# Optimization experiments

Hardware: AMD Instinct MI355X
Metric: run time of the kernel (lower is better)

## Reference

```python
import jax, jax.numpy as jnp
import numpy as np

N = 100_000   # nodes
E = 3_200_000 # edges
G = 128       # graphs in batch
H = 32        # hidden_dim
PI = float(np.pi)


def setup_inputs() -> dict:
    key = jax.random.key(0)
    ks = jax.random.split(key, 18)
    p = lambda k, s: (jax.random.normal(k, s, dtype=jnp.float32) * 0.1)
    x = jax.random.normal(ks[0], (N, 1), dtype=jnp.float32)
    edge_index = jax.random.randint(ks[1], (2, E), 0, N, dtype=jnp.int32)
    batch = jnp.sort(jax.random.randint(ks[2], (N,), 0, G, dtype=jnp.int32))
    return dict(
        x=x, edge_index=edge_index, batch=batch,
        W1=p(ks[3], (1, H)),  b1=jnp.zeros((H,), jnp.float32),
        W2=p(ks[4], (H, H)),  b2=jnp.zeros((H,), jnp.float32),
        W3=p(ks[5], (H, H)),  b3=jnp.zeros((H,), jnp.float32),
        Wt1=p(ks[6], (H, 32)), bt1=jnp.zeros((32,), jnp.float32),
        Wt2=p(ks[7], (32, 1)), bt2=jnp.zeros((1,), jnp.float32),
        Wg1=p(ks[8], (H, 32)), bg1=jnp.zeros((32,), jnp.float32),
        Wg2=p(ks[9], (32, 2)), bg2=jnp.zeros((2,), jnp.float32),
    )


def _gcn_norm(edge_index):
    # PyG GCNConv default: add self-loops, symmetric normalization.
    loop = jnp.arange(N, dtype=edge_index.dtype)
    src = jnp.concatenate([edge_index[0], loop])
    dst = jnp.concatenate([edge_index[1], loop])
    deg = jax.ops.segment_sum(jnp.ones_like(dst, dtype=jnp.float32), dst, num_segments=N)
    dinv = jnp.where(deg > 0, jax.lax.rsqrt(jnp.maximum(deg, 1.0)), 0.0)
    norm = dinv[src] * dinv[dst]  # [E+N]
    return src, dst, norm


def _gcn_conv(x, W, b, src, dst, norm):
    h = x @ W                                  # [N, out]
    msg = h[src] * norm[:, None]               # gather + scale  [E+N, out]
    return jax.ops.segment_sum(msg, dst, num_segments=N) + b


def _forward(x, W1, b1, W2, b2, W3, b3, Wt1, bt1, Wt2, bt2, Wg1, bg1, Wg2, bg2,
             edge_index, batch):
    src, dst, norm = _gcn_norm(edge_index)
    x = jax.nn.relu(_gcn_conv(x, W1, b1, src, dst, norm))
    x = jax.nn.relu(_gcn_conv(x, W2, b2, src, dst, norm))
    h = jax.nn.relu(_gcn_conv(x, W3, b3, src, dst, norm))
    # theta head per node
    theta = PI * jax.nn.sigmoid(jax.nn.relu(h @ Wt1 + bt1) @ Wt2 + bt2)[:, 0]  # [N]
    # global mean pool per graph
    counts = jax.ops.segment_sum(jnp.ones((N,), jnp.float32), batch, num_segments=G)
    gsum = jax.ops.segment_sum(h, batch, num_segments=G)
    gemb = gsum / jnp.maximum(counts, 1.0)[:, None]                            # [G, H]
    beta_gamma = 2.0 * PI * jax.nn.sigmoid(jax.nn.relu(gemb @ Wg1 + bg1) @ Wg2 + bg2)  # [G, 2]
    return theta, beta_gamma


def reference(x, edge_index, batch, W1, b1, W2, b2, W3, b3,
              Wt1, bt1, Wt2, bt2, Wg1, bg1, Wg2, bg2):
    return _forward(x, W1, b1, W2, b2, W3, b3, Wt1, bt1, Wt2, bt2,
                    Wg1, bg1, Wg2, bg2, edge_index, batch)
```

## Files before the change

### kernel.cpp

```cpp
#include <hip/hip_runtime.h>
#include <hip/hip_bf16.h>

#define PI_F 3.14159265358979323846f
#define NBLK 256
#define BSH 8
#define BSZ 256
#define SCAP 10240

static inline size_t align256(size_t x) { return (x + 255) & ~size_t(255); }

typedef float v2f __attribute__((ext_vector_type(2)));

__device__ __forceinline__ unsigned bfpack(float a, float b) {
    unsigned lo = (__float_as_uint(a) + 0x8000u) >> 16;
    unsigned hi = (__float_as_uint(b) + 0x8000u) & 0xFFFF0000u;
    return lo | hi;
}

__device__ __forceinline__ void f8acc(uint2 q, float rs, float acc[8]) {
    v2f l0 = __builtin_amdgcn_cvt_pk_f32_fp8(q.x, false);
    v2f h0 = __builtin_amdgcn_cvt_pk_f32_fp8(q.x, true);
    v2f l1 = __builtin_amdgcn_cvt_pk_f32_fp8(q.y, false);
    v2f h1 = __builtin_amdgcn_cvt_pk_f32_fp8(q.y, true);
    acc[0] += rs * l0.x; acc[1] += rs * l0.y; acc[2] += rs * h0.x; acc[3] += rs * h0.y;
    acc[4] += rs * l1.x; acc[5] += rs * l1.y; acc[6] += rs * h1.x; acc[7] += rs * h1.y;
}


__global__ void __launch_bounds__(1024) count_kernel(
                             const int* __restrict__ dst, int* __restrict__ C,
                             int E, int CHUNK, int NB2) {
    extern __shared__ int hist[];
    for (int i = threadIdx.x; i < NB2; i += 1024) hist[i] = 0;
    __syncthreads();
    int s0 = blockIdx.x * CHUNK, s1 = min(s0 + CHUNK, E);
    for (int e = s0 + threadIdx.x; e < s1; e += 1024)
        atomicAdd(&hist[dst[e] >> BSH], 1);
    __syncthreads();
    for (int i = threadIdx.x; i < NB2; i += 1024)
        C[(size_t)blockIdx.x * NB2 + i] = hist[i];
}

__global__ void scan_blocks_kernel(int* __restrict__ C, int* __restrict__ colsum, int NB2) {
    __shared__ int s[256];
    int k = blockIdx.x;
    int b = threadIdx.x;
    int v = C[(size_t)b * NB2 + k];
    s[b] = v;
    __syncthreads();
    for (int off = 1; off < 256; off <<= 1) {
        int w = (b >= off) ? s[b - off] : 0;
        __syncthreads();
        s[b] += w;
        __syncthreads();
    }
    C[(size_t)b * NB2 + k] = s[b] - v;
    if (b == 255) colsum[k] = s[255];
}

__global__ void scan_totals_kernel(const int* __restrict__ colsum, int* __restrict__ bbase,
                                   int NB2, int E) {
    __shared__ int s[256];
    __shared__ int running;
    if (threadIdx.x == 0) running = 0;
    __syncthreads();
    for (int base = 0; base < NB2; base += 256) {
        int i = base + threadIdx.x;
        int v = (i < NB2) ? colsum[i] : 0;
        s[threadIdx.x] = v;
        __syncthreads();
        for (int off = 1; off < 256; off <<= 1) {
            int w = (threadIdx.x >= (unsigned)off) ? s[threadIdx.x - off] : 0;
            __syncthreads();
            s[threadIdx.x] += w;
            __syncthreads();
        }
        if (i < NB2) bbase[i] = running + s[threadIdx.x] - v;
        __syncthreads();
        if (threadIdx.x == 255) running += s[255];
        __syncthreads();
    }
    if (threadIdx.x == 0) bbase[NB2] = E;
}

__global__ void __launch_bounds__(1024) scatter_kernel(
                               const int* __restrict__ src, const int* __restrict__ dst,
                               const int* __restrict__ C, const int* __restrict__ bbase,
                               unsigned* __restrict__ bkt_data, int E, int CHUNK, int NB2) {
    extern __shared__ int ofs[];
    for (int i = threadIdx.x; i < NB2; i += 1024)
        ofs[i] = bbase[i] + C[(size_t)blockIdx.x * NB2 + i];
    __syncthreads();
    int s0 = blockIdx.x * CHUNK, s1 = min(s0 + CHUNK, E);
    for (int e = s0 + threadIdx.x; e < s1; e += 1024) {
        int d = dst[e];
        int p = atomicAdd(&ofs[d >> BSH], 1);
        bkt_data[p] = ((unsigned)(d & (BSZ - 1)) << 17) | (unsigned)src[e];
    }
}

__global__ void __launch_bounds__(512) csr_build_kernel(
                                 const unsigned* __restrict__ bkt_data, const int* __restrict__ bbase,
                                 const float* __restrict__ x,
                                 unsigned* __restrict__ csr, int* __restrict__ e_start,
                                 float* __restrict__ dinv, float* __restrict__ xd,
                                 int N, int NB2) {
    __shared__ unsigned sdata[SCAP];
    __shared__ int hist[256];
    __shared__ int scn[256];
    __shared__ int bump[256];
    int tid = threadIdx.x;
    int b = blockIdx.x;
    int g0 = bbase[b], g1 = bbase[b + 1];
    int cnt = g1 - g0;
    bool fits = (cnt <= SCAP);
    if (tid < 256) hist[tid] = 0;
    __syncthreads();
    for (int i = tid; i < cnt; i += 512) {
        unsigned pk = bkt_data[g0 + i];
        if (fits) sdata[i] = pk;
        atomicAdd(&hist[pk >> 17], 1);
    }
    __syncthreads();
    int orig = (tid < 256) ? hist[tid] : 0;
    if (tid < 256) scn[tid] = orig;
    __syncthreads();
    for (int off = 1; off < 256; off <<= 1) {
        int w = (tid >= off && tid < 256) ? scn[tid - off] : 0;
        __syncthreads();
        if (tid < 256) scn[tid] += w;
        __syncthreads();
    }
    if (tid < 256) {
        int excl = scn[tid] - orig;
        bump[tid] = g0 + excl;
        int node = b * BSZ + tid;
        if (node < N) {
            float dv = rsqrtf((float)(orig + 1));
            dinv[node] = dv;
            xd[node] = x[node] * dv;
            e_start[node] = g0 + excl;
        }
    }
    if (b == NB2 - 1 && tid == 0) e_start[N] = g1;
    __syncthreads();
    for (int i = tid; i < cnt; i += 512) {
        unsigned pk = fits ? sdata[i] : bkt_data[g0 + i];
        int p = atomicAdd(&bump[pk >> 17], 1);
        csr[p] = pk & 0x1FFFFu;
    }
}


__device__ __forceinline__ void mm32_8(const float* __restrict__ sW, const float vr[8],
                                       int sub, int lane, float o[8]) {
    const float4* sW4 = (const float4*)sW;
    int base = lane & ~3;
#pragma unroll
    for (int r = 0; r < 4; r++) {
#pragma unroll
        for (int i = 0; i < 8; i++) {
            float vk = __shfl(vr[i], base | r, 64);
            int k = r * 8 + i;
            float4 w0 = sW4[k * 8 + sub * 2];
            float4 w1 = sW4[k * 8 + sub * 2 + 1];
            o[0] += vk * w0.x; o[1] += vk * w0.y; o[2] += vk * w0.z; o[3] += vk * w0.w;
            o[4] += vk * w1.x; o[5] += vk * w1.y; o[6] += vk * w1.z; o[7] += vk * w1.w;
        }
    }
}

__device__ __forceinline__ void store_f8(unsigned char* __restrict__ u8, float* __restrict__ uscale,
                                         int d, int sub, const float o[8]) {
    float am = 0.f;
#pragma unroll
    for (int i = 0; i < 8; i++) am = fmaxf(am, fabsf(o[i]));
    am = fmaxf(am, __shfl_xor(am, 1, 64));
    am = fmaxf(am, __shfl_xor(am, 2, 64));
    float rm = fmaxf(am, 1e-20f);
    float sc = 128.f / rm;
    unsigned w0 = 0, w1 = 0;
    w0 = __builtin_amdgcn_cvt_pk_fp8_f32(o[0] * sc, o[1] * sc, w0, false);
    w0 = __builtin_amdgcn_cvt_pk_fp8_f32(o[2] * sc, o[3] * sc, w0, true);
    w1 = __builtin_amdgcn_cvt_pk_fp8_f32(o[4] * sc, o[5] * sc, w1, false);
    w1 = __builtin_amdgcn_cvt_pk_fp8_f32(o[6] * sc, o[7] * sc, w1, true);
    uint2 st; st.x = w0; st.y = w1;
    ((uint2*)u8)[(size_t)d * 4 + sub] = st;
    if (sub == 0) uscale[d] = rm * (1.f / 128.f);
}

__global__ void __launch_bounds__(256) agg1_kernel(
                            const float* __restrict__ xd, const int* __restrict__ e_start,
                            const unsigned* __restrict__ csr, const float* __restrict__ dinv,
                            const float* __restrict__ W1, const float* __restrict__ b1,
                            const float* __restrict__ W2,
                            unsigned char* __restrict__ u8o, float* __restrict__ uso, int n) {
    __shared__ float sW2[1024];
    __shared__ float sW1[32], sb1[32];
    for (int i = threadIdx.x; i < 1024; i += 256) sW2[i] = W2[i];
    if (threadIdx.x < 32) { sW1[threadIdx.x] = W1[threadIdx.x]; sb1[threadIdx.x] = b1[threadIdx.x]; }
    __syncthreads();
    int t = blockIdx.x * 256 + threadIdx.x;
    int d = t >> 2, sub = t & 3;
    int lane = threadIdx.x & 63;
    if (d >= n) return;
    int e0 = e_start[d];
    int cnt = e_start[d + 1] - e0;
    float s = 0.f;
    int j = sub;
    for (; j + 8 <= cnt; j += 8) {
        int i0 = (int)csr[e0 + j], i1 = (int)csr[e0 + j + 4];
        s += xd[i0]; s += xd[i1];
    }
    for (; j < cnt; j += 4) s += xd[(int)csr[e0 + j]];
    s += __shfl_xor(s, 1, 64);
    s += __shfl_xor(s, 2, 64);
    float dv = dinv[d];
    float tt = dv * (s + xd[d]);
    float vr[8];
#pragma unroll
    for (int i = 0; i < 8; i++) vr[i] = fmaxf(tt * sW1[sub * 8 + i] + sb1[sub * 8 + i], 0.f);
    float o[8];
#pragma unroll
    for (int i = 0; i < 8; i++) o[i] = 0.f;
    mm32_8(sW2, vr, sub, lane, o);
#pragma unroll
    for (int i = 0; i < 8; i++) o[i] *= dv;
    store_f8(u8o, uso, d, sub, o);
}

__device__ __forceinline__ void gather_f8(const unsigned char* __restrict__ u8,
                                          const float* __restrict__ uscale,
                                          const unsigned* __restrict__ csr,
                                          int e0, int cnt, int d, int sub, float acc[8]) {
#pragma unroll
    for (int i = 0; i < 8; i++) acc[i] = 0.f;
    const uint2* rows = (const uint2*)u8;
    int j = 0;
    for (; j + 4 <= cnt; j += 4) {
        int i0 = (int)csr[e0 + j],     i1 = (int)csr[e0 + j + 1];
        int i2 = (int)csr[e0 + j + 2], i3 = (int)csr[e0 + j + 3];
        float r0 = uscale[i0], r1 = uscale[i1], r2 = uscale[i2], r3 = uscale[i3];
        uint2 q0 = rows[(size_t)i0 * 4 + sub];
        uint2 q1 = rows[(size_t)i1 * 4 + sub];
        uint2 q2 = rows[(size_t)i2 * 4 + sub];
        uint2 q3 = rows[(size_t)i3 * 4 + sub];
        f8acc(q0, r0, acc); f8acc(q1, r1, acc); f8acc(q2, r2, acc); f8acc(q3, r3, acc);
    }
    for (; j < cnt; j++) {
        int i0 = (int)csr[e0 + j];
        float r0 = uscale[i0];
        uint2 q0 = rows[(size_t)i0 * 4 + sub];
        f8acc(q0, r0, acc);
    }
    float rs = uscale[d];
    uint2 qs = rows[(size_t)d * 4 + sub];
    f8acc(qs, rs, acc);
}

__global__ void __launch_bounds__(256) agg2_kernel(
                            const unsigned char* __restrict__ u8, const float* __restrict__ uscale,
                            const int* __restrict__ e_start, const unsigned* __restrict__ csr,
                            const float* __restrict__ dinv, const float* __restrict__ bias,
                            const float* __restrict__ W,
                            unsigned char* __restrict__ o8, float* __restrict__ oscale, int n) {
    __shared__ float sW[1024];
    __shared__ float sb[32];
    for (int i = threadIdx.x; i < 1024; i += 256) sW[i] = W[i];
    if (threadIdx.x < 32) sb[threadIdx.x] = bias[threadIdx.x];
    __syncthreads();
    int t = blockIdx.x * 256 + threadIdx.x;
    int d = t >> 2, sub = t & 3;
    int lane = threadIdx.x & 63;
    if (d >= n) return;
    int e0 = e_start[d];
    int cnt = e_start[d + 1] - e0;
    float acc[8];
    gather_f8(u8, uscale, csr, e0, cnt, d, sub, acc);
    float dv = dinv[d];
    float vr[8];
#pragma unroll
    for (int i = 0; i < 8; i++) vr[i] = fmaxf(dv * acc[i] + sb[sub * 8 + i], 0.f);
    float o[8];
#pragma unroll
    for (int i = 0; i < 8; i++) o[i] = 0.f;
    mm32_8(sW, vr, sub, lane, o);
#pragma unroll
    for (int i = 0; i < 8; i++) o[i] *= dv;
    store_f8(o8, oscale, d, sub, o);
}

__global__ void __launch_bounds__(256) agg3_kernel(
                            const unsigned char* __restrict__ u8, const float* __restrict__ uscale,
                            const int* __restrict__ e_start, const unsigned* __restrict__ csr,
                            const float* __restrict__ dinv, const float* __restrict__ bias,
                            const float* __restrict__ Wt1, const float* __restrict__ bt1,
                            const float* __restrict__ Wt2, const float* __restrict__ bt2,
                            unsigned short* __restrict__ hb, float* __restrict__ theta, int n) {
    __shared__ float sW[1024];
    __shared__ float sb[32], sbt[32], sw2[32];
    for (int i = threadIdx.x; i < 1024; i += 256) sW[i] = Wt1[i];
    if (threadIdx.x < 32) {
        sb[threadIdx.x] = bias[threadIdx.x];
        sbt[threadIdx.x] = bt1[threadIdx.x];
        sw2[threadIdx.x] = Wt2[threadIdx.x];
    }
    __syncthreads();
    int t = blockIdx.x * 256 + threadIdx.x;
    int d = t >> 2, sub = t & 3;
    int lane = threadIdx.x & 63;
    if (d >= n) return;
    int e0 = e_start[d];
    int cnt = e_start[d + 1] - e0;
    float acc[8];
    gather_f8(u8, uscale, csr, e0, cnt, d, sub, acc);
    float dv = dinv[d];
    float vr[8];
#pragma unroll
    for (int i = 0; i < 8; i++) vr[i] = fmaxf(dv * acc[i] + sb[sub * 8 + i], 0.f);
    unsigned ow[4];
#pragma unroll
    for (int i2 = 0; i2 < 4; i2++) ow[i2] = bfpack(vr[2 * i2], vr[2 * i2 + 1]);
    ((uint4*)hb)[(size_t)d * 4 + sub] = *(uint4*)&ow[0];
    float o[8];
#pragma unroll
    for (int i = 0; i < 8; i++) o[i] = 0.f;
    mm32_8(sW, vr, sub, lane, o);
    float tl = 0.f;
#pragma unroll
    for (int i = 0; i < 8; i++)
        tl += fmaxf(o[i] + sbt[sub * 8 + i], 0.f) * sw2[sub * 8 + i];
    tl += __shfl_xor(tl, 1, 64);
    tl += __shfl_xor(tl, 2, 64);
    if (sub == 0) theta[d] = PI_F / (1.f + __expf(-(tl + bt2[0])));
}


__global__ void gb_kernel(const int* __restrict__ batch, int* __restrict__ gstart,
                          int n, int G) {
    int i = blockIdx.x * 256 + threadIdx.x;
    if (i >= n) return;
    int g = batch[i];
    if (i == 0) {
        for (int gg = 0; gg <= g; gg++) gstart[gg] = 0;
    } else {
        int gp = batch[i - 1];
        for (int gg = gp + 1; gg <= g; gg++) gstart[gg] = i;
    }
    if (i == n - 1) {
        for (int gg = g + 1; gg <= G; gg++) gstart[gg] = n;
    }
}

__global__ void __launch_bounds__(512) bg_kernel(
                          const unsigned short* __restrict__ hb, const int* __restrict__ gstart,
                          const float* __restrict__ Wg1, const float* __restrict__ bg1v,
                          const float* __restrict__ Wg2, const float* __restrict__ bg2v,
                          float* __restrict__ out, int G) {
    __shared__ float sW[1024];
    __shared__ float part[8][32];
    for (int i = threadIdx.x; i < 1024; i += 512) sW[i] = Wg1[i];
    int g = blockIdx.x;
    int s = gstart[g], e = gstart[g + 1];
    int w = threadIdx.x >> 6;
    int lane = threadIdx.x & 63;
    int f = lane & 31, h = lane >> 5;
    float a = 0.f;
    for (int i = s + (w << 1) + h; i < e; i += 16)
        a += __uint_as_float((unsigned)hb[((size_t)i << 5) + f] << 16);
    a += __shfl_xor(a, 32, 64);
    if (h == 0) part[w][f] = a;
    __syncthreads();
    if (w == 0) {
        float hv = 0.f;
#pragma unroll
        for (int p = 0; p < 8; p++) hv += part[p][f];
        hv /= fmaxf((float)(e - s), 1.f);
        int base = lane & 32;
        float acc = bg1v[f];
#pragma unroll
        for (int k = 0; k < 32; k++) acc += __shfl(hv, base | k, 64) * sW[k * 32 + f];
        acc = fmaxf(acc, 0.f);
        float p0 = acc * Wg2[f * 2 + 0];
        float p1 = acc * Wg2[f * 2 + 1];
#pragma unroll
        for (int m = 1; m < 32; m <<= 1) {
            p0 += __shfl_xor(p0, m, 64);
            p1 += __shfl_xor(p1, m, 64);
        }
        if (lane == 0) {
            out[g * 2 + 0] = 2.f * PI_F / (1.f + __expf(-(p0 + bg2v[0])));
            out[g * 2 + 1] = 2.f * PI_F / (1.f + __expf(-(p1 + bg2v[1])));
        }
    }
}


extern "C" void kernel_launch(void* const* d_in, const int* in_sizes, int n_in,
                              void* d_out, int out_size, void* d_ws, size_t ws_size,
                              hipStream_t stream) {
    const float* x   = (const float*)d_in[0];
    const int*   ei  = (const int*)d_in[1];
    const int* batch = (const int*)d_in[2];
    const float* W1  = (const float*)d_in[3];
    const float* b1  = (const float*)d_in[4];
    const float* W2  = (const float*)d_in[5];
    const float* b2  = (const float*)d_in[6];
    const float* W3  = (const float*)d_in[7];
    const float* b3  = (const float*)d_in[8];
    const float* Wt1 = (const float*)d_in[9];
    const float* bt1 = (const float*)d_in[10];
    const float* Wt2 = (const float*)d_in[11];
    const float* bt2 = (const float*)d_in[12];
    const float* Wg1 = (const float*)d_in[13];
    const float* bg1 = (const float*)d_in[14];
    const float* Wg2 = (const float*)d_in[15];
    const float* bg2 = (const float*)d_in[16];

    const int N = in_sizes[0];
    const int E = in_sizes[1] / 2;
    const int G = 128;
    const int* src = ei;
    const int* dst = ei + E;
    float* theta_out = (float*)d_out;
    float* bg_out = (float*)d_out + N;

    const int NB2 = (N + BSZ - 1) >> BSH;
    const int CHUNK = (E + NBLK - 1) / NBLK;

    char* w = (char*)d_ws;
    auto alloc = [&](size_t bytes) -> char* { char* p = w; w += align256(bytes); return p; };
    int*      C        = (int*)alloc((size_t)NBLK * NB2 * 4);
    int*      colsum   = (int*)alloc((size_t)NB2 * 4);
    int*      bbase    = (int*)alloc((size_t)(NB2 + 1) * 4);
    unsigned* bkt_data = (unsigned*)alloc((size_t)E * 4);
    unsigned* csr      = (unsigned*)alloc((size_t)E * 4);
    int*      e_start  = (int*)alloc((size_t)(N + 1) * 4);
    float*    dinv     = (float*)alloc((size_t)N * 4);
    float*    xd       = (float*)alloc((size_t)N * 4);
    unsigned char* u2  = (unsigned char*)alloc((size_t)N * 32);
    float*    us2      = (float*)alloc((size_t)N * 4);
    unsigned char* u3  = (unsigned char*)alloc((size_t)N * 32);
    float*    us3      = (float*)alloc((size_t)N * 4);
    unsigned short* hb = (unsigned short*)alloc((size_t)N * 64);
    int*      gstart   = (int*)alloc((size_t)(G + 1) * 4);

    size_t ldsB = (size_t)NB2 * 4;
    count_kernel<<<NBLK, 1024, ldsB, stream>>>(dst, C, E, CHUNK, NB2);
    scan_blocks_kernel<<<NB2, 256, 0, stream>>>(C, colsum, NB2);
    scan_totals_kernel<<<1, 256, 0, stream>>>(colsum, bbase, NB2, E);
    scatter_kernel<<<NBLK, 1024, ldsB, stream>>>(src, dst, C, bbase, bkt_data, E, CHUNK, NB2);
    csr_build_kernel<<<NB2, 512, 0, stream>>>(bkt_data, bbase, x, csr, e_start, dinv, xd, N, NB2);
    gb_kernel<<<(N + 255) / 256, 256, 0, stream>>>(batch, gstart, N, G);

    unsigned gridQ = (unsigned)(((size_t)N * 4 + 255) / 256);

    agg1_kernel<<<gridQ, 256, 0, stream>>>(xd, e_start, csr, dinv, W1, b1, W2, u2, us2, N);
    agg2_kernel<<<gridQ, 256, 0, stream>>>(u2, us2, e_start, csr, dinv, b2, W3, u3, us3, N);
    agg3_kernel<<<gridQ, 256, 0, stream>>>(u3, us3, e_start, csr, dinv, b3,
                                           Wt1, bt1, Wt2, bt2, hb, theta_out, N);

    bg_kernel<<<G, 512, 0, stream>>>(hb, gstart, Wg1, bg1, Wg2, bg2, bg_out, G);
}
```

Before: 287.8 us.

## Stage per-block CSR neighbor indices in LDS for aggregation kernels

Each aggregation kernel block now loads the contiguous CSR index range for its 64 destination nodes into shared memory with nontemporal loads, then gathers neighbors from LDS indices instead of re-reading global CSR per thread. The fp8 gather loop is unrolled to 8 neighbors to raise memory-level parallelism, with a fallback to the old global path when the range exceeds the LDS capacity. Output stores of hb and theta use nontemporal hints. It adds 12KB of LDS per block, which can reduce occupancy, and an extra barrier.

```diff
diff --git a/kernel.cpp b/kernel.cpp
--- a/kernel.cpp
+++ b/kernel.cpp
@@ -6,10 +6,12 @@
 #define BSH 8
 #define BSZ 256
 #define SCAP 10240
+#define SLDS 3072
 
 static inline size_t align256(size_t x) { return (x + 255) & ~size_t(255); }
 
 typedef float v2f __attribute__((ext_vector_type(2)));
+typedef unsigned uvec4 __attribute__((ext_vector_type(4)));
 
 __device__ __forceinline__ unsigned bfpack(float a, float b) {
     unsigned lo = (__float_as_uint(a) + 0x8000u) >> 16;
@@ -189,6 +191,21 @@
     if (sub == 0) uscale[d] = rm * (1.f / 128.f);
 }
 
+__device__ __forceinline__ bool stage_csr(const unsigned* __restrict__ csr,
+                                          const int* __restrict__ e_start,
+                                          int d0, int dEnd, int* sidx, int& E0) {
+    E0 = e_start[d0];
+    int E1 = e_start[dEnd];
+    int m = E1 - E0;
+    bool fits = (m <= SLDS);
+    if (fits) {
+        for (int i = threadIdx.x; i < m; i += 256)
+            sidx[i] = (int)__builtin_nontemporal_load(&csr[E0 + i]);
+    }
+    __syncthreads();
+    return fits;
+}
+
 __global__ void __launch_bounds__(256) agg1_kernel(
                             const float* __restrict__ xd, const int* __restrict__ e_start,
                             const unsigned* __restrict__ csr, const float* __restrict__ dinv,
@@ -197,22 +214,26 @@
                             unsigned char* __restrict__ u8o, float* __restrict__ uso, int n) {
     __shared__ float sW2[1024];
     __shared__ float sW1[32], sb1[32];
+    __shared__ int sidx[SLDS];
     for (int i = threadIdx.x; i < 1024; i += 256) sW2[i] = W2[i];
     if (threadIdx.x < 32) { sW1[threadIdx.x] = W1[threadIdx.x]; sb1[threadIdx.x] = b1[threadIdx.x]; }
-    __syncthreads();
-    int t = blockIdx.x * 256 + threadIdx.x;
-    int d = t >> 2, sub = t & 3;
+    int d0 = blockIdx.x * 64;
+    int dEnd = min(d0 + 64, n);
+    int E0;
+    bool fits = stage_csr(csr, e_start, d0, dEnd, sidx, E0);
+    int d = d0 + (threadIdx.x >> 2), sub = threadIdx.x & 3;
     int lane = threadIdx.x & 63;
     if (d >= n) return;
     int e0 = e_start[d];
     int cnt = e_start[d + 1] - e0;
+    int l0 = e0 - E0;
     float s = 0.f;
     int j = sub;
-    for (; j + 8 <= cnt; j += 8) {
-        int i0 = (int)csr[e0 + j], i1 = (int)csr[e0 + j + 4];
-        s += xd[i0]; s += xd[i1];
-    }
-    for (; j < cnt; j += 4) s += xd[(int)csr[e0 + j]];
+    if (fits) {
+        for (; j < cnt; j += 4) s += xd[sidx[l0 + j]];
+    } else {
+        for (; j < cnt; j += 4) s += xd[(int)csr[e0 + j]];
+    }
     s += __shfl_xor(s, 1, 64);
     s += __shfl_xor(s, 2, 64);
     float dv = dinv[d];
@@ -231,31 +252,48 @@
 
 __device__ __forceinline__ void gather_f8(const unsigned char* __restrict__ u8,
                                           const float* __restrict__ uscale,
+                                          const int* __restrict__ sidx, bool fits,
                                           const unsigned* __restrict__ csr,
-                                          int e0, int cnt, int d, int sub, float acc[8]) {
+                                          int e0, int l0, int cnt, int d, int sub, float acc[8]) {
 #pragma unroll
     for (int i = 0; i < 8; i++) acc[i] = 0.f;
     const uint2* rows = (const uint2*)u8;
     int j = 0;
-    for (; j + 4 <= cnt; j += 4) {
-        int i0 = (int)csr[e0 + j],     i1 = (int)csr[e0 + j + 1];
-        int i2 = (int)csr[e0 + j + 2], i3 = (int)csr[e0 + j + 3];
-        float r0 = uscale[i0], r1 = uscale[i1], r2 = uscale[i2], r3 = uscale[i3];
-        uint2 q0 = rows[(size_t)i0 * 4 + sub];
-        uint2 q1 = rows[(size_t)i1 * 4 + sub];
-        uint2 q2 = rows[(size_t)i2 * 4 + sub];
-        uint2 q3 = rows[(size_t)i3 * 4 + sub];
-        f8acc(q0, r0, acc); f8acc(q1, r1, acc); f8acc(q2, r2, acc); f8acc(q3, r3, acc);
-    }
-    for (; j < cnt; j++) {
-        int i0 = (int)csr[e0 + j];
-        float r0 = uscale[i0];
-        uint2 q0 = rows[(size_t)i0 * 4 + sub];
-        f8acc(q0, r0, acc);
-    }
-    float rs = uscale[d];
-    uint2 qs = rows[(size_t)d * 4 + sub];
-    f8acc(qs, rs, acc);
+    if (fits) {
+        for (; j + 8 <= cnt; j += 8) {
+            int id[8];
+#pragma unroll
+            for (int k = 0; k < 8; k++) id[k] = sidx[l0 + j + k];
+            float rs[8];
+#pragma unroll
+            for (int k = 0; k < 8; k++) rs[k] = uscale[id[k]];
+            uint2 q[8];
+#pragma unroll
+            for (int k = 0; k < 8; k++) q[k] = rows[(size_t)id[k] * 4 + sub];
+#pragma unroll
+            for (int k = 0; k < 8; k++) f8acc(q[k], rs[k], acc);
+        }
+        for (; j < cnt; j++) {
+            int i0 = sidx[l0 + j];
+            f8acc(rows[(size_t)i0 * 4 + sub], uscale[i0], acc);
+        }
+    } else {
+        for (; j + 4 <= cnt; j += 4) {
+            int i0 = (int)csr[e0 + j],     i1 = (int)csr[e0 + j + 1];
+            int i2 = (int)csr[e0 + j + 2], i3 = (int)csr[e0 + j + 3];
+            float r0 = uscale[i0], r1 = uscale[i1], r2 = uscale[i2], r3 = uscale[i3];
+            uint2 q0 = rows[(size_t)i0 * 4 + sub];
+            uint2 q1 = rows[(size_t)i1 * 4 + sub];
+            uint2 q2 = rows[(size_t)i2 * 4 + sub];
+            uint2 q3 = rows[(size_t)i3 * 4 + sub];
+            f8acc(q0, r0, acc); f8acc(q1, r1, acc); f8acc(q2, r2, acc); f8acc(q3, r3, acc);
+        }
+        for (; j < cnt; j++) {
+            int i0 = (int)csr[e0 + j];
+            f8acc(rows[(size_t)i0 * 4 + sub], uscale[i0], acc);
+        }
+    }
+    f8acc(rows[(size_t)d * 4 + sub], uscale[d], acc);
 }
 
 __global__ void __launch_bounds__(256) agg2_kernel(
@@ -266,17 +304,20 @@
                             unsigned char* __restrict__ o8, float* __restrict__ oscale, int n) {
     __shared__ float sW[1024];
     __shared__ float sb[32];
+    __shared__ int sidx[SLDS];
     for (int i = threadIdx.x; i < 1024; i += 256) sW[i] = W[i];
     if (threadIdx.x < 32) sb[threadIdx.x] = bias[threadIdx.x];
-    __syncthreads();
-    int t = blockIdx.x * 256 + threadIdx.x;
-    int d = t >> 2, sub = t & 3;
+    int d0 = blockIdx.x * 64;
+    int dEnd = min(d0 + 64, n);
+    int E0;
+    bool fits = stage_csr(csr, e_start, d0, dEnd, sidx, E0);
+    int d = d0 + (threadIdx.x >> 2), sub = threadIdx.x & 3;
     int lane = threadIdx.x & 63;
     if (d >= n) return;
     int e0 = e_start[d];
     int cnt = e_start[d + 1] - e0;
     float acc[8];
-    gather_f8(u8, uscale, csr, e0, cnt, d, sub, acc);
+    gather_f8(u8, uscale, sidx, fits, csr, e0, e0 - E0, cnt, d, sub, acc);
     float dv = dinv[d];
     float vr[8];
 #pragma unroll
@@ -299,29 +340,34 @@
                             unsigned short* __restrict__ hb, float* __restrict__ theta, int n) {
     __shared__ float sW[1024];
     __shared__ float sb[32], sbt[32], sw2[32];
+    __shared__ int sidx[SLDS];
     for (int i = threadIdx.x; i < 1024; i += 256) sW[i] = Wt1[i];
     if (threadIdx.x < 32) {
         sb[threadIdx.x] = bias[threadIdx.x];
         sbt[threadIdx.x] = bt1[threadIdx.x];
         sw2[threadIdx.x] = Wt2[threadIdx.x];
     }
-    __syncthreads();
-    int t = blockIdx.x * 256 + threadIdx.x;
-    int d = t >> 2, sub = t & 3;
+    int d0 = blockIdx.x * 64;
+    int dEnd = min(d0 + 64, n);
+    int E0;
+    bool fits = stage_csr(csr, e_start, d0, dEnd, sidx, E0);
+    int d = d0 + (threadIdx.x >> 2), sub = threadIdx.x & 3;
     int lane = threadIdx.x & 63;
     if (d >= n) return;
     int e0 = e_start[d];
     int cnt = e_start[d + 1] - e0;
     float acc[8];
-    gather_f8(u8, uscale, csr, e0, cnt, d, sub, acc);
+    gather_f8(u8, uscale, sidx, fits, csr, e0, e0 - E0, cnt, d, sub, acc);
     float dv = dinv[d];
     float vr[8];
 #pragma unroll
     for (int i = 0; i < 8; i++) vr[i] = fmaxf(dv * acc[i] + sb[sub * 8 + i], 0.f);
-    unsigned ow[4];
-#pragma unroll
-    for (int i2 = 0; i2 < 4; i2++) ow[i2] = bfpack(vr[2 * i2], vr[2 * i2 + 1]);
-    ((uint4*)hb)[(size_t)d * 4 + sub] = *(uint4*)&ow[0];
+    uvec4 st;
+    st.x = bfpack(vr[0], vr[1]);
+    st.y = bfpack(vr[2], vr[3]);
+    st.z = bfpack(vr[4], vr[5]);
+    st.w = bfpack(vr[6], vr[7]);
+    __builtin_nontemporal_store(st, (uvec4*)hb + (size_t)d * 4 + sub);
     float o[8];
 #pragma unroll
     for (int i = 0; i < 8; i++) o[i] = 0.f;
@@ -332,7 +378,7 @@
         tl += fmaxf(o[i] + sbt[sub * 8 + i], 0.f) * sw2[sub * 8 + i];
     tl += __shfl_xor(tl, 1, 64);
     tl += __shfl_xor(tl, 2, 64);
-    if (sub == 0) theta[d] = PI_F / (1.f + __expf(-(tl + bt2[0])));
+    if (sub == 0) __builtin_nontemporal_store(PI_F / (1.f + __expf(-(tl + bt2[0]))), theta + d);
 }
 
 
```

Result: no change. 282.2 us (-1.9%).
